# Kernel optimization log

Hardware: AMD Instinct MI355X
Metric: run time of the kernel (lower is better)

Reference implementation:

```python
import jax, jax.numpy as jnp
import numpy as np

B, N, D = 16, 2048, 64

def setup_inputs() -> dict:
    key = jax.random.key(0)
    kq, kk, kv = jax.random.split(key, 3)
    queries = jax.random.normal(kq, (B, N, D), dtype=jnp.float32)
    keys = jax.random.normal(kk, (B, N, D), dtype=jnp.float32)
    values = jax.random.normal(kv, (B, N, D), dtype=jnp.float32)
    scaling_factor = jnp.asarray(np.sqrt(D), dtype=jnp.float32)
    return {"queries": queries, "keys": keys, "values": values, "scaling_factor": scaling_factor}

def reference(queries, keys, values, scaling_factor):
    # scores: [B, N, N] = Q K^T / scale
    scores = jnp.einsum('bqd,bkd->bqk', queries, keys) / scaling_factor
    atn = jax.nn.softmax(scores, axis=2)
    return jnp.einsum('bqk,bkd->bqd', atn, values)
```

## Files before the change

kernel.cpp:

```cpp
#include <hip/hip_runtime.h>
#include <hip/hip_bf16.h>

#define BATCH 16
#define SEQ 2048
#define DIM 64

typedef __attribute__((ext_vector_type(8))) __bf16 bf16x8;
typedef __attribute__((ext_vector_type(8))) unsigned short u16x8;
typedef __attribute__((ext_vector_type(4))) unsigned int u32x4;
typedef __attribute__((ext_vector_type(16))) float f32x16;

#if __has_builtin(__builtin_amdgcn_exp2f)
#define EXP2F(x) __builtin_amdgcn_exp2f(x)
#else
#define EXP2F(x) __expf(0.69314718055994531f * (x))
#endif

__device__ __forceinline__ unsigned short f2bf_hw(float f) {
    __bf16 h = (__bf16)f;
    return __builtin_bit_cast(unsigned short, h);
}

__device__ __forceinline__ unsigned int pk_bf16(float lo, float hi) {
    unsigned int a = f2bf_hw(lo), b = f2bf_hw(hi);
    return a | (b << 16);
}

__device__ __forceinline__ bf16x8 ld_bf8_g(const unsigned short* p) {
    u16x8 u = *(const u16x8*)p;
    return __builtin_bit_cast(bf16x8, u);
}

__global__ __launch_bounds__(256)
void preconvert_kv(const float* __restrict__ K, const float* __restrict__ V,
                   unsigned short* __restrict__ Ks, unsigned short* __restrict__ Vts) {
    __shared__ float vt[128 * 65];
    const int tid = threadIdx.x;
    const int b = blockIdx.x >> 4;
    const int t = blockIdx.x & 15;
    const int kt = t * 128;

    {
        const float* src = V + ((size_t)(b * SEQ + kt)) * DIM;
        #pragma unroll
        for (int p = 0; p < 8; ++p) {
            const int f = p * 256 + tid;
            const int row = f >> 4, c4 = (f & 15) << 2;
            float4 x = *(const float4*)(src + row * DIM + c4);
            vt[row * 65 + c4 + 0] = x.x; vt[row * 65 + c4 + 1] = x.y;
            vt[row * 65 + c4 + 2] = x.z; vt[row * 65 + c4 + 3] = x.w;
        }
    }
    {
        const float* src = K + ((size_t)(b * SEQ + kt)) * DIM;
        unsigned short* dst = Ks + ((size_t)(b * 16 + t)) * 8192;
        #pragma unroll
        for (int p = 0; p < 4; ++p) {
            const int cid = p * 256 + tid;
            const int key = cid >> 3, g = cid & 7;
            const int d0 = (g >> 1) * 16 + (g & 1) * 8;
            float4 x0 = *(const float4*)(src + key * DIM + d0);
            float4 x1 = *(const float4*)(src + key * DIM + d0 + 4);
            u16x8 o;
            o[0] = f2bf_hw(x0.x); o[1] = f2bf_hw(x0.y); o[2] = f2bf_hw(x0.z); o[3] = f2bf_hw(x0.w);
            o[4] = f2bf_hw(x1.x); o[5] = f2bf_hw(x1.y); o[6] = f2bf_hw(x1.z); o[7] = f2bf_hw(x1.w);
            *(u16x8*)(dst + (g * 128 + key) * 8) = o;
        }
    }
    __syncthreads();
    {
        unsigned short* dst = Vts + ((size_t)(b * 16 + t)) * 8192;
        #pragma unroll
        for (int p = 0; p < 4; ++p) {
            const int cid = p * 256 + tid;
            const int g = cid >> 6, d = cid & 63;
            const int k0 = (g >> 1) * 16 + (g & 1) * 8;
            u16x8 o;
            #pragma unroll
            for (int j = 0; j < 8; ++j) o[j] = f2bf_hw(vt[(k0 + j) * 65 + d]);
            *(u16x8*)(dst + (g * 64 + d) * 8) = o;
        }
    }
}

__global__ __launch_bounds__(256, 4)
void attn_flash_kernel(const float* __restrict__ Q,
                       const unsigned short* __restrict__ Ks,
                       const unsigned short* __restrict__ Vts,
                       const float* __restrict__ scaling,
                       float* __restrict__ O) {
    __shared__ float comb[3 * 64 * 33];

    const int tid  = threadIdx.x;
    const int w    = tid >> 6;
    const int lane = tid & 63;
    const int m    = lane & 31;
    const int h    = lane >> 5;

    const int x  = blockIdx.x;
    const int b  = ((x & 7) << 1) | ((x >> 3) & 1);
    const int q0 = (x >> 4) * 32;

    const float csc = 1.4426950408889634f / scaling[0];

    bf16x8 aq[4];
    {
        const float* qsrc = Q + ((size_t)(b * SEQ + q0 + m)) * DIM + h * 8;
        #pragma unroll
        for (int c = 0; c < 4; ++c) {
            float4 x0 = *(const float4*)(qsrc + c * 16);
            float4 x1 = *(const float4*)(qsrc + c * 16 + 4);
            u32x4 pk;
            pk[0] = pk_bf16(x0.x * csc, x0.y * csc);
            pk[1] = pk_bf16(x0.z * csc, x0.w * csc);
            pk[2] = pk_bf16(x1.x * csc, x1.y * csc);
            pk[3] = pk_bf16(x1.z * csc, x1.w * csc);
            aq[c] = __builtin_bit_cast(bf16x8, pk);
        }
    }

    f32x16 Oacc[2];
    #pragma unroll
    for (int dt = 0; dt < 2; ++dt)
        #pragma unroll
        for (int r = 0; r < 16; ++r) Oacc[dt][r] = 0.f;
    float psum = 0.f;

    const unsigned short* Kbase = Ks + ((size_t)(b * 16 + w * 4)) * 8192;
    const unsigned short* Vbase = Vts + ((size_t)(b * 16 + w * 4)) * 8192;

    for (int it = 0; it < 4; ++it) {
        const unsigned short* Kt = Kbase + (size_t)it * 8192;
        const unsigned short* Vt = Vbase + (size_t)it * 8192;
        #pragma unroll
        for (int t = 0; t < 4; ++t) {
            f32x16 S;
            #pragma unroll
            for (int r = 0; r < 16; ++r) S[r] = 0.f;
            #pragma unroll
            for (int c = 0; c < 4; ++c) {
                bf16x8 bk = ld_bf8_g(&Kt[((c * 2 + h) * 128 + t * 32 + m) * 8]);
                S = __builtin_amdgcn_mfma_f32_32x32x16_bf16(bk, aq[c], S, 0, 0, 0);
            }
            unsigned int d0[8], ds[8];
            float ps = 0.f;
            #pragma unroll
            for (int k = 0; k < 4; ++k) {
                float p0 = EXP2F(S[4 * k + 0]);
                float p1 = EXP2F(S[4 * k + 1]);
                float p2 = EXP2F(S[4 * k + 2]);
                float p3 = EXP2F(S[4 * k + 3]);
                ps += (p0 + p1) + (p2 + p3);
                d0[2 * k + 0] = pk_bf16(p0, p1);
                d0[2 * k + 1] = pk_bf16(p2, p3);
            }
            psum += ps;
            #pragma unroll
            for (int i = 0; i < 8; ++i) ds[i] = (unsigned int)__shfl_xor((int)d0[i], 32);
            #pragma unroll
            for (int c2 = 0; c2 < 2; ++c2) {
                u32x4 bw;
                bw[0] = h ? ds[4 * c2 + 2] : d0[4 * c2 + 0];
                bw[1] = h ? ds[4 * c2 + 3] : d0[4 * c2 + 1];
                bw[2] = h ? d0[4 * c2 + 2] : ds[4 * c2 + 0];
                bw[3] = h ? d0[4 * c2 + 3] : ds[4 * c2 + 1];
                bf16x8 pb = __builtin_bit_cast(bf16x8, bw);
                const int kc = 2 * t + c2;
                #pragma unroll
                for (int dt = 0; dt < 2; ++dt) {
                    bf16x8 bv = ld_bf8_g(&Vt[((kc * 2 + h) * 64 + dt * 32 + m) * 8]);
                    Oacc[dt] = __builtin_amdgcn_mfma_f32_32x32x16_bf16(bv, pb, Oacc[dt], 0, 0, 0);
                }
            }
        }
    }

    float lq = psum + __shfl_xor(psum, 32);
    if (w > 0) {
        float* dst = comb + ((w - 1) * 64 + lane) * 33;
        #pragma unroll
        for (int dt = 0; dt < 2; ++dt)
            #pragma unroll
            for (int r = 0; r < 16; ++r) dst[dt * 16 + r] = Oacc[dt][r];
        dst[32] = lq;
    }
    __syncthreads();
    if (w == 0) {
        const float* p0 = comb + (0 * 64 + lane) * 33;
        const float* p1 = comb + (1 * 64 + lane) * 33;
        const float* p2 = comb + (2 * 64 + lane) * 33;
        const float invl = 1.0f / (lq + p0[32] + p1[32] + p2[32]);
        float* orow = O + ((size_t)(b * SEQ + q0 + m)) * DIM;
        #pragma unroll
        for (int dt = 0; dt < 2; ++dt) {
            #pragma unroll
            for (int k = 0; k < 4; ++k) {
                float4 o4;
                #pragma unroll
                for (int j = 0; j < 4; ++j) {
                    const int r = 4 * k + j;
                    ((float*)&o4)[j] = (Oacc[dt][r] + p0[dt * 16 + r] + p1[dt * 16 + r]
                                        + p2[dt * 16 + r]) * invl;
                }
                *(float4*)(orow + dt * 32 + 8 * k + 4 * h) = o4;
            }
        }
    }
}

extern "C" void kernel_launch(void* const* d_in, const int* in_sizes, int n_in,
                              void* d_out, int out_size, void* d_ws, size_t ws_size,
                              hipStream_t stream) {
    const float* Q = (const float*)d_in[0];
    const float* K = (const float*)d_in[1];
    const float* V = (const float*)d_in[2];
    const float* scaling = (const float*)d_in[3];
    float* O = (float*)d_out;

    unsigned short* Ks  = (unsigned short*)d_ws;
    unsigned short* Vts = Ks + (size_t)BATCH * 16 * 8192;

    preconvert_kv<<<dim3(BATCH * 16), dim3(256), 0, stream>>>(K, V, Ks, Vts);
    attn_flash_kernel<<<dim3(BATCH * (SEQ / 32)), dim3(256), 0, stream>>>(Q, Ks, Vts, scaling, O);
}
```

Baseline: 126.2 us.

## Process two 32-row query tiles per block to reuse K/V loads

Each block now handles 64 query rows as two 32-row sub-tiles that share every K and V fragment load, halving global/L2 traffic per query. The grid shrinks to 512 blocks, and launch bounds drop to 2 blocks per CU to make room for the doubled accumulators and score registers. The LDS combine buffer doubles to hold both sub-tiles. The cost is higher register pressure and fewer blocks to spread across the CUs, with about two waves' worth of work on 256 CUs.

```diff
diff --git a/kernel.cpp b/kernel.cpp
--- a/kernel.cpp
+++ b/kernel.cpp
@@ -83,13 +83,13 @@
     }
 }
 
-__global__ __launch_bounds__(256, 4)
+__global__ __launch_bounds__(256, 2)
 void attn_flash_kernel(const float* __restrict__ Q,
                        const unsigned short* __restrict__ Ks,
                        const unsigned short* __restrict__ Vts,
                        const float* __restrict__ scaling,
                        float* __restrict__ O) {
-    __shared__ float comb[3 * 64 * 33];
+    __shared__ float comb[3 * 64 * 66];
 
     const int tid  = threadIdx.x;
     const int w    = tid >> 6;
@@ -99,13 +99,14 @@
 
     const int x  = blockIdx.x;
     const int b  = ((x & 7) << 1) | ((x >> 3) & 1);
-    const int q0 = (x >> 4) * 32;
+    const int q0 = (x >> 4) * 64;
 
     const float csc = 1.4426950408889634f / scaling[0];
 
-    bf16x8 aq[4];
-    {
-        const float* qsrc = Q + ((size_t)(b * SEQ + q0 + m)) * DIM + h * 8;
+    bf16x8 aq0[4], aq1[4];
+    #pragma unroll
+    for (int s = 0; s < 2; ++s) {
+        const float* qsrc = Q + ((size_t)(b * SEQ + q0 + s * 32 + m)) * DIM + h * 8;
         #pragma unroll
         for (int c = 0; c < 4; ++c) {
             float4 x0 = *(const float4*)(qsrc + c * 16);
@@ -115,16 +116,16 @@
             pk[1] = pk_bf16(x0.z * csc, x0.w * csc);
             pk[2] = pk_bf16(x1.x * csc, x1.y * csc);
             pk[3] = pk_bf16(x1.z * csc, x1.w * csc);
-            aq[c] = __builtin_bit_cast(bf16x8, pk);
-        }
-    }
-
-    f32x16 Oacc[2];
+            (s ? aq1 : aq0)[c] = __builtin_bit_cast(bf16x8, pk);
+        }
+    }
+
+    f32x16 Oacc0[2], Oacc1[2];
     #pragma unroll
     for (int dt = 0; dt < 2; ++dt)
         #pragma unroll
-        for (int r = 0; r < 16; ++r) Oacc[dt][r] = 0.f;
-    float psum = 0.f;
+        for (int r = 0; r < 16; ++r) { Oacc0[dt][r] = 0.f; Oacc1[dt][r] = 0.f; }
+    float psum0 = 0.f, psum1 = 0.f;
 
     const unsigned short* Kbase = Ks + ((size_t)(b * 16 + w * 4)) * 8192;
     const unsigned short* Vbase = Vts + ((size_t)(b * 16 + w * 4)) * 8192;
@@ -134,63 +135,81 @@
         const unsigned short* Vt = Vbase + (size_t)it * 8192;
         #pragma unroll
         for (int t = 0; t < 4; ++t) {
-            f32x16 S;
-            #pragma unroll
-            for (int r = 0; r < 16; ++r) S[r] = 0.f;
+            f32x16 S0, S1;
+            #pragma unroll
+            for (int r = 0; r < 16; ++r) { S0[r] = 0.f; S1[r] = 0.f; }
             #pragma unroll
             for (int c = 0; c < 4; ++c) {
                 bf16x8 bk = ld_bf8_g(&Kt[((c * 2 + h) * 128 + t * 32 + m) * 8]);
-                S = __builtin_amdgcn_mfma_f32_32x32x16_bf16(bk, aq[c], S, 0, 0, 0);
-            }
-            unsigned int d0[8], ds[8];
-            float ps = 0.f;
+                S0 = __builtin_amdgcn_mfma_f32_32x32x16_bf16(bk, aq0[c], S0, 0, 0, 0);
+                S1 = __builtin_amdgcn_mfma_f32_32x32x16_bf16(bk, aq1[c], S1, 0, 0, 0);
+            }
+            unsigned int d0a[8], d0b[8], dsa[8], dsb[8];
             #pragma unroll
             for (int k = 0; k < 4; ++k) {
-                float p0 = EXP2F(S[4 * k + 0]);
-                float p1 = EXP2F(S[4 * k + 1]);
-                float p2 = EXP2F(S[4 * k + 2]);
-                float p3 = EXP2F(S[4 * k + 3]);
-                ps += (p0 + p1) + (p2 + p3);
-                d0[2 * k + 0] = pk_bf16(p0, p1);
-                d0[2 * k + 1] = pk_bf16(p2, p3);
-            }
-            psum += ps;
-            #pragma unroll
-            for (int i = 0; i < 8; ++i) ds[i] = (unsigned int)__shfl_xor((int)d0[i], 32);
+                float a0 = EXP2F(S0[4 * k + 0]), a1 = EXP2F(S0[4 * k + 1]);
+                float a2 = EXP2F(S0[4 * k + 2]), a3 = EXP2F(S0[4 * k + 3]);
+                psum0 += (a0 + a1) + (a2 + a3);
+                d0a[2 * k + 0] = pk_bf16(a0, a1);
+                d0a[2 * k + 1] = pk_bf16(a2, a3);
+                float b0 = EXP2F(S1[4 * k + 0]), b1 = EXP2F(S1[4 * k + 1]);
+                float b2 = EXP2F(S1[4 * k + 2]), b3 = EXP2F(S1[4 * k + 3]);
+                psum1 += (b0 + b1) + (b2 + b3);
+                d0b[2 * k + 0] = pk_bf16(b0, b1);
+                d0b[2 * k + 1] = pk_bf16(b2, b3);
+            }
+            #pragma unroll
+            for (int i = 0; i < 8; ++i) {
+                dsa[i] = (unsigned int)__shfl_xor((int)d0a[i], 32);
+                dsb[i] = (unsigned int)__shfl_xor((int)d0b[i], 32);
+            }
             #pragma unroll
             for (int c2 = 0; c2 < 2; ++c2) {
-                u32x4 bw;
-                bw[0] = h ? ds[4 * c2 + 2] : d0[4 * c2 + 0];
-                bw[1] = h ? ds[4 * c2 + 3] : d0[4 * c2 + 1];
-                bw[2] = h ? d0[4 * c2 + 2] : ds[4 * c2 + 0];
-                bw[3] = h ? d0[4 * c2 + 3] : ds[4 * c2 + 1];
-                bf16x8 pb = __builtin_bit_cast(bf16x8, bw);
+                u32x4 bw0, bw1;
+                bw0[0] = h ? dsa[4 * c2 + 2] : d0a[4 * c2 + 0];
+                bw0[1] = h ? dsa[4 * c2 + 3] : d0a[4 * c2 + 1];
+                bw0[2] = h ? d0a[4 * c2 + 2] : dsa[4 * c2 + 0];
+                bw0[3] = h ? d0a[4 * c2 + 3] : dsa[4 * c2 + 1];
+                bw1[0] = h ? dsb[4 * c2 + 2] : d0b[4 * c2 + 0];
+                bw1[1] = h ? dsb[4 * c2 + 3] : d0b[4 * c2 + 1];
+                bw1[2] = h ? d0b[4 * c2 + 2] : dsb[4 * c2 + 0];
+                bw1[3] = h ? d0b[4 * c2 + 3] : dsb[4 * c2 + 1];
+                bf16x8 pb0 = __builtin_bit_cast(bf16x8, bw0);
+                bf16x8 pb1 = __builtin_bit_cast(bf16x8, bw1);
                 const int kc = 2 * t + c2;
                 #pragma unroll
                 for (int dt = 0; dt < 2; ++dt) {
                     bf16x8 bv = ld_bf8_g(&Vt[((kc * 2 + h) * 64 + dt * 32 + m) * 8]);
-                    Oacc[dt] = __builtin_amdgcn_mfma_f32_32x32x16_bf16(bv, pb, Oacc[dt], 0, 0, 0);
+                    Oacc0[dt] = __builtin_amdgcn_mfma_f32_32x32x16_bf16(bv, pb0, Oacc0[dt], 0, 0, 0);
+                    Oacc1[dt] = __builtin_amdgcn_mfma_f32_32x32x16_bf16(bv, pb1, Oacc1[dt], 0, 0, 0);
                 }
             }
         }
     }
 
-    float lq = psum + __shfl_xor(psum, 32);
+    float l0 = psum0 + __shfl_xor(psum0, 32);
+    float l1 = psum1 + __shfl_xor(psum1, 32);
     if (w > 0) {
-        float* dst = comb + ((w - 1) * 64 + lane) * 33;
+        float* dst = comb + ((w - 1) * 64 + lane) * 66;
         #pragma unroll
         for (int dt = 0; dt < 2; ++dt)
             #pragma unroll
-            for (int r = 0; r < 16; ++r) dst[dt * 16 + r] = Oacc[dt][r];
-        dst[32] = lq;
+            for (int r = 0; r < 16; ++r) {
+                dst[dt * 16 + r]      = Oacc0[dt][r];
+                dst[33 + dt * 16 + r] = Oacc1[dt][r];
+            }
+        dst[32] = l0;
+        dst[65] = l1;
     }
     __syncthreads();
     if (w == 0) {
-        const float* p0 = comb + (0 * 64 + lane) * 33;
-        const float* p1 = comb + (1 * 64 + lane) * 33;
-        const float* p2 = comb + (2 * 64 + lane) * 33;
-        const float invl = 1.0f / (lq + p0[32] + p1[32] + p2[32]);
-        float* orow = O + ((size_t)(b * SEQ + q0 + m)) * DIM;
+        const float* p0 = comb + (0 * 64 + lane) * 66;
+        const float* p1 = comb + (1 * 64 + lane) * 66;
+        const float* p2 = comb + (2 * 64 + lane) * 66;
+        const float invl0 = 1.0f / (l0 + p0[32] + p1[32] + p2[32]);
+        const float invl1 = 1.0f / (l1 + p0[65] + p1[65] + p2[65]);
+        float* orow0 = O + ((size_t)(b * SEQ + q0 + m)) * DIM;
+        float* orow1 = O + ((size_t)(b * SEQ + q0 + 32 + m)) * DIM;
         #pragma unroll
         for (int dt = 0; dt < 2; ++dt) {
             #pragma unroll
@@ -199,10 +218,17 @@
                 #pragma unroll
                 for (int j = 0; j < 4; ++j) {
                     const int r = 4 * k + j;
-                    ((float*)&o4)[j] = (Oacc[dt][r] + p0[dt * 16 + r] + p1[dt * 16 + r]
-                                        + p2[dt * 16 + r]) * invl;
+                    ((float*)&o4)[j] = (Oacc0[dt][r] + p0[dt * 16 + r] + p1[dt * 16 + r]
+                                        + p2[dt * 16 + r]) * invl0;
                 }
-                *(float4*)(orow + dt * 32 + 8 * k + 4 * h) = o4;
+                *(float4*)(orow0 + dt * 32 + 8 * k + 4 * h) = o4;
+                #pragma unroll
+                for (int j = 0; j < 4; ++j) {
+                    const int r = 4 * k + j;
+                    ((float*)&o4)[j] = (Oacc1[dt][r] + p0[33 + dt * 16 + r] + p1[33 + dt * 16 + r]
+                                        + p2[33 + dt * 16 + r]) * invl1;
+                }
+                *(float4*)(orow1 + dt * 32 + 8 * k + 4 * h) = o4;
             }
         }
     }
@@ -221,5 +247,5 @@
     unsigned short* Vts = Ks + (size_t)BATCH * 16 * 8192;
 
     preconvert_kv<<<dim3(BATCH * 16), dim3(256), 0, stream>>>(K, V, Ks, Vts);
-    attn_flash_kernel<<<dim3(BATCH * (SEQ / 32)), dim3(256), 0, stream>>>(Q, Ks, Vts, scaling, O);
-}
+    attn_flash_kernel<<<dim3(BATCH * (SEQ / 64)), dim3(256), 0, stream>>>(Q, Ks, Vts, scaling, O);
+}
```

Result: faster. 107.5 us (-14.8%).
